# Optimization experiments

Hardware: AMD Instinct MI355X
Metric: run time of the kernel (lower is better)

The kernel has to match this reference:

```python
import jax, jax.numpy as jnp
import numpy as np

IMG = 64
FS = 96
NH = 6          # num_head == channel dim C (forced by LayerNorm(num_head))
B = 8
HW = IMG * IMG  # 4096
FF = FS * FS    # 9216, Mlp in/hidden features
EPS = 1e-5


def setup_inputs() -> dict:
    key = jax.random.key(0)
    ks = jax.random.split(key, 7)
    x = jax.random.normal(ks[0], (B, NH, HW), jnp.float32)
    feature = jax.random.normal(ks[1], (B, NH, FF), jnp.float32)
    s1 = 1.0 / np.sqrt(FF)
    fc1_w = jax.random.uniform(ks[2], (FF, FF), jnp.float32, -s1, s1)
    fc1_b = jax.random.uniform(ks[3], (FF,), jnp.float32, -s1, s1)
    fc2_w = jax.random.uniform(ks[4], (HW, FF), jnp.float32, -s1, s1)
    fc2_b = jax.random.uniform(ks[5], (HW,), jnp.float32, -s1, s1)
    logit_scale = jnp.log(10.0 * jnp.ones((1, 1, HW), jnp.float32))
    norm_w = jnp.ones((NH,), jnp.float32)
    norm_b = jnp.zeros((NH,), jnp.float32)
    return {"x": x, "feature": feature, "fc1_w": fc1_w, "fc1_b": fc1_b,
            "fc2_w": fc2_w, "fc2_b": fc2_b, "logit_scale": logit_scale,
            "norm_w": norm_w, "norm_b": norm_b}


def reference(x, feature, fc1_w, fc1_b, fc2_w, fc2_b, logit_scale, norm_w, norm_b):
    # x: [B, C, HW]; feature: [B, C, FF]
    xt = jnp.swapaxes(x, 1, 2)                                  # [B, HW, C]
    # Mlp (ReLU act, drop=0): FF -> FF -> HW
    h = jax.nn.relu(jnp.einsum('bcf,hf->bch', feature, fc1_w) + fc1_b)
    f = jnp.einsum('bch,oh->bco', h, fc2_w) + fc2_b             # [B, C, HW]
    # cosine-style logit scale, clamped at log(1/0.01)
    max_log = jnp.log(jnp.float32(100.0))
    ls = jnp.exp(jnp.minimum(logit_scale, max_log))             # [1, 1, HW]
    temp = jnp.einsum('bnc,bcm->bnm', xt, f) * ls               # [B, HW, HW]
    temp = jax.nn.softmax(temp, axis=1)                         # softmax over dim 1
    out = jnp.einsum('bnm,bmc->bnc', temp, xt)                  # [B, HW, C]
    # LayerNorm over last dim (C == num_head), biased variance, eps=1e-5
    mu = jnp.mean(out, axis=-1, keepdims=True)
    var = jnp.mean((out - mu) ** 2, axis=-1, keepdims=True)
    out = (out - mu) / jnp.sqrt(var + EPS) * norm_w + norm_b
    return jnp.swapaxes(out, 1, 2)                              # [B, C, HW]
```

## Files before the change

### kernel.cpp

```cpp
#include <hip/hip_runtime.h>
#include <math.h>

#define BATCH 8
#define CH 6
#define HW 4096
#define FF 9216
#define RC 48
#define LOG2E 1.44269504088896340736f
#define LN100 4.6051701859880913680f

__global__ __launch_bounds__(256) void prep_kernel(
    const float* __restrict__ x, const float* __restrict__ feature,
    float* __restrict__ featT, float* __restrict__ xT)
{
    int i = blockIdx.x * 256 + threadIdx.x;
    if (i < FF * RC) {
        int k = i / RC, r = i - k * RC;
        featT[i] = feature[(size_t)r * FF + k];
    } else {
        int t = i - FF * RC;
        if (t < BATCH * HW * CH) {
            int c = t % CH;
            int n = (t / CH) & (HW - 1);
            int b = t / (HW * CH);
            xT[t] = x[((size_t)(b * CH + c)) * HW + n];
        }
    }
}

__global__ __launch_bounds__(256) void gemm48(
    const float* __restrict__ W, const float* __restrict__ AT,
    float* __restrict__ part, int K, int kchunk)
{
    __shared__ float ldsW[32 * 128];
    __shared__ float ldsA[32 * 48];
    const int t = threadIdx.x;
    const int tx = t & 31;
    const int ty = t >> 5;
    const int j0 = blockIdx.x * 128;
    const int kbase = blockIdx.y * kchunk;
    const int ntiles = kchunk >> 5;

    const int wrow = t >> 3;
    const int wk4  = (t & 7) * 4;

    float acc[4][6];
#pragma unroll
    for (int q = 0; q < 4; ++q)
#pragma unroll
        for (int i = 0; i < 6; ++i) acc[q][i] = 0.f;

    for (int tile = 0; tile < ntiles; ++tile) {
        const int kt = kbase + tile * 32;
#pragma unroll
        for (int rnd = 0; rnd < 4; ++rnd) {
            int row = rnd * 32 + wrow;
            float4 v = *(const float4*)(W + (size_t)(j0 + row) * K + kt + wk4);
            float* dst = ldsW + rnd * 32;
            dst[(wk4 + 0) * 128 + (wrow ^ (wk4 + 0))] = v.x;
            dst[(wk4 + 1) * 128 + (wrow ^ (wk4 + 1))] = v.y;
            dst[(wk4 + 2) * 128 + (wrow ^ (wk4 + 2))] = v.z;
            dst[(wk4 + 3) * 128 + (wrow ^ (wk4 + 3))] = v.w;
        }
        {
            const float2* asrc = (const float2*)(AT + (size_t)kt * RC);
            float2* adst = (float2*)ldsA;
            adst[t]       = asrc[t];
            adst[t + 256] = asrc[t + 256];
            adst[t + 512] = asrc[t + 512];
        }
        __syncthreads();
#pragma unroll 4
        for (int k = 0; k < 32; ++k) {
            const float* wr = ldsW + k * 128;
            int js = tx ^ k;
            float w0 = wr[js];
            float w1 = wr[32 + js];
            float w2 = wr[64 + js];
            float w3 = wr[96 + js];
            const float* ar = ldsA + k * RC + 6 * ty;
            float a0 = ar[0], a1 = ar[1], a2 = ar[2];
            float a3 = ar[3], a4 = ar[4], a5 = ar[5];
            acc[0][0] = fmaf(w0, a0, acc[0][0]);
            acc[0][1] = fmaf(w0, a1, acc[0][1]);
            acc[0][2] = fmaf(w0, a2, acc[0][2]);
            acc[0][3] = fmaf(w0, a3, acc[0][3]);
            acc[0][4] = fmaf(w0, a4, acc[0][4]);
            acc[0][5] = fmaf(w0, a5, acc[0][5]);
            acc[1][0] = fmaf(w1, a0, acc[1][0]);
            acc[1][1] = fmaf(w1, a1, acc[1][1]);
            acc[1][2] = fmaf(w1, a2, acc[1][2]);
            acc[1][3] = fmaf(w1, a3, acc[1][3]);
            acc[1][4] = fmaf(w1, a4, acc[1][4]);
            acc[1][5] = fmaf(w1, a5, acc[1][5]);
            acc[2][0] = fmaf(w2, a0, acc[2][0]);
            acc[2][1] = fmaf(w2, a1, acc[2][1]);
            acc[2][2] = fmaf(w2, a2, acc[2][2]);
            acc[2][3] = fmaf(w2, a3, acc[2][3]);
            acc[2][4] = fmaf(w2, a4, acc[2][4]);
            acc[2][5] = fmaf(w2, a5, acc[2][5]);
            acc[3][0] = fmaf(w3, a0, acc[3][0]);
            acc[3][1] = fmaf(w3, a1, acc[3][1]);
            acc[3][2] = fmaf(w3, a2, acc[3][2]);
            acc[3][3] = fmaf(w3, a3, acc[3][3]);
            acc[3][4] = fmaf(w3, a4, acc[3][4]);
            acc[3][5] = fmaf(w3, a5, acc[3][5]);
        }
        __syncthreads();
    }

    const int N = gridDim.x * 128;
    float* base = part + ((size_t)blockIdx.y * N + j0) * RC + 6 * ty;
#pragma unroll
    for (int q = 0; q < 4; ++q) {
        float* dst = base + (size_t)(q * 32 + tx) * RC;
        float2 v0 = make_float2(acc[q][0], acc[q][1]);
        float2 v1 = make_float2(acc[q][2], acc[q][3]);
        float2 v2 = make_float2(acc[q][4], acc[q][5]);
        *(float2*)(dst + 0) = v0;
        *(float2*)(dst + 2) = v1;
        *(float2*)(dst + 4) = v2;
    }
}

__global__ __launch_bounds__(256) void reduce_relu(
    const float* __restrict__ part, const float* __restrict__ bias,
    float* __restrict__ hT, int nchunks)
{
    int i = blockIdx.x * 256 + threadIdx.x;
    const int total = FF * RC;
    if (i >= total) return;
    float s = 0.f;
    for (int c = 0; c < nchunks; ++c) s += part[(size_t)c * total + i];
    int j = i / RC;
    s += bias[j];
    hT[i] = fmaxf(s, 0.f);
}

__global__ __launch_bounds__(256) void reduce_scale(
    const float* __restrict__ part, const float* __restrict__ bias,
    const float* __restrict__ logit_scale, float* __restrict__ fTs, int nchunks)
{
    int i = blockIdx.x * 256 + threadIdx.x;
    const int total = HW * RC;
    if (i >= total) return;
    float s = 0.f;
    for (int c = 0; c < nchunks; ++c) s += part[(size_t)c * total + i];
    int m = i / RC, rc = i - m * RC;
    int b = rc / CH, cc = rc - b * CH;
    float lv = fminf(logit_scale[m], LN100);
    float ls = __builtin_amdgcn_exp2f(lv * LOG2E);
    s = (s + bias[m]) * ls * LOG2E;
    fTs[((size_t)b * HW + m) * CH + cc] = s;
}

__global__ __launch_bounds__(256) void colsum_kernel(
    const float* __restrict__ fTs, const float* __restrict__ xT,
    float* __restrict__ Dpart)
{
    __shared__ float xs[512 * CH];
    const int t = threadIdx.x;
    const int b = blockIdx.y;
    const int ns = blockIdx.z;
    {
        const float4* src = (const float4*)(xT + ((size_t)b * HW + ns * 512) * CH);
        float4* dst = (float4*)xs;
        dst[t]       = src[t];
        dst[t + 256] = src[t + 256];
        dst[t + 512] = src[t + 512];
    }
    __syncthreads();

    int m = blockIdx.x * 256 + t;
    const float2* f2 = (const float2*)(fTs + ((size_t)b * HW + m) * CH);
    float2 fa = f2[0], fb = f2[1], fc = f2[2];
    float s0 = fa.x, s1 = fa.y, s2 = fb.x, s3 = fb.y, s4 = fc.x, s5 = fc.y;

    float D = 0.f;
#pragma unroll 4
    for (int n = 0; n < 512; ++n) {
        const float* xn = xs + n * CH;
        float a = fmaf(s0, xn[0], fmaf(s1, xn[1], fmaf(s2, xn[2],
                  fmaf(s3, xn[3], fmaf(s4, xn[4], s5 * xn[5])))));
        D += __builtin_amdgcn_exp2f(a);
    }
    Dpart[((size_t)b * 8 + ns) * HW + m] = D;
}

__global__ __launch_bounds__(256) void combineD_kernel(
    const float* __restrict__ Dpart, const float* __restrict__ xT,
    float* __restrict__ xR)
{
    int i = blockIdx.x * 256 + threadIdx.x;
    if (i >= BATCH * HW) return;
    int b = i >> 12, m = i & (HW - 1);
    float s = 0.f;
    for (int ns = 0; ns < 8; ++ns) s += Dpart[((size_t)b * 8 + ns) * HW + m];
    float r = 1.0f / s;
    const float2* xs = (const float2*)(xT + (size_t)i * CH);
    float2 v0 = xs[0], v1 = xs[1], v2 = xs[2];
    float2* xd = (float2*)(xR + (size_t)i * CH);
    xd[0] = make_float2(v0.x * r, v0.y * r);
    xd[1] = make_float2(v1.x * r, v1.y * r);
    xd[2] = make_float2(v2.x * r, v2.y * r);
}

__global__ __launch_bounds__(256) void attn_out_kernel(
    const float* __restrict__ fTs, const float* __restrict__ xT,
    const float* __restrict__ xR, const float* __restrict__ nw,
    const float* __restrict__ nb, float* __restrict__ out)
{
    int b = blockIdx.y;
    int wv = threadIdx.x >> 6;
    int lane = threadIdx.x & 63;
    int n0 = (blockIdx.x * 4 + wv) * 8;

    const float* __restrict__ xb = xT + (size_t)b * HW * CH;
    float xn[8][6];
#pragma unroll
    for (int n = 0; n < 8; ++n)
#pragma unroll
        for (int c = 0; c < 6; ++c) xn[n][c] = xb[(size_t)(n0 + n) * CH + c];

    const float* __restrict__ frb = fTs + (size_t)b * HW * CH;
    const float* __restrict__ xrb = xR + (size_t)b * HW * CH;

    float acc[8][6];
#pragma unroll
    for (int n = 0; n < 8; ++n)
#pragma unroll
        for (int c = 0; c < 6; ++c) acc[n][c] = 0.f;

    for (int i = 0; i < 64; ++i) {
        int m = i * 64 + lane;
        const float2* f2 = (const float2*)(frb + (size_t)m * CH);
        float2 fa = f2[0], fb = f2[1], fc = f2[2];
        const float2* x2 = (const float2*)(xrb + (size_t)m * CH);
        float2 xa = x2[0], xb2 = x2[1], xc = x2[2];
        float f0 = fa.x, f1 = fa.y, f2v = fb.x, f3 = fb.y, f4 = fc.x, f5 = fc.y;
#pragma unroll
        for (int n = 0; n < 8; ++n) {
            float a = fmaf(f0, xn[n][0], fmaf(f1, xn[n][1], fmaf(f2v, xn[n][2],
                      fmaf(f3, xn[n][3], fmaf(f4, xn[n][4], f5 * xn[n][5])))));
            float p = __builtin_amdgcn_exp2f(a);
            acc[n][0] = fmaf(p, xa.x, acc[n][0]);
            acc[n][1] = fmaf(p, xa.y, acc[n][1]);
            acc[n][2] = fmaf(p, xb2.x, acc[n][2]);
            acc[n][3] = fmaf(p, xb2.y, acc[n][3]);
            acc[n][4] = fmaf(p, xc.x, acc[n][4]);
            acc[n][5] = fmaf(p, xc.y, acc[n][5]);
        }
    }

#pragma unroll
    for (int n = 0; n < 8; ++n)
#pragma unroll
        for (int c = 0; c < 6; ++c) {
            float v = acc[n][c];
            for (int d = 1; d < 64; d <<= 1) v += __shfl_xor(v, d, 64);
            acc[n][c] = v;
        }

    if (lane == 0) {
        float wc[6], bc[6];
#pragma unroll
        for (int c = 0; c < 6; ++c) { wc[c] = nw[c]; bc[c] = nb[c]; }
#pragma unroll
        for (int n = 0; n < 8; ++n) {
            float mu = (acc[n][0] + acc[n][1] + acc[n][2] +
                        acc[n][3] + acc[n][4] + acc[n][5]) * (1.f / 6.f);
            float var = 0.f;
#pragma unroll
            for (int c = 0; c < 6; ++c) {
                float dv = acc[n][c] - mu;
                var = fmaf(dv, dv, var);
            }
            var *= (1.f / 6.f);
            float inv = rsqrtf(var + 1e-5f);
#pragma unroll
            for (int c = 0; c < 6; ++c)
                out[((size_t)(b * CH + c)) * HW + n0 + n] =
                    (acc[n][c] - mu) * inv * wc[c] + bc[c];
        }
    }
}

extern "C" void kernel_launch(void* const* d_in, const int* in_sizes, int n_in,
                              void* d_out, int out_size, void* d_ws, size_t ws_size,
                              hipStream_t stream)
{
    const float* x           = (const float*)d_in[0];
    const float* feature     = (const float*)d_in[1];
    const float* fc1_w       = (const float*)d_in[2];
    const float* fc1_b       = (const float*)d_in[3];
    const float* fc2_w       = (const float*)d_in[4];
    const float* fc2_b       = (const float*)d_in[5];
    const float* logit_scale = (const float*)d_in[6];
    const float* norm_w      = (const float*)d_in[7];
    const float* norm_b      = (const float*)d_in[8];
    float* out = (float*)d_out;

    float* ws = (float*)d_ws;
    float* featT = ws;
    float* hT    = featT + 442368;
    float* p1    = hT    + 442368;
    float* p2    = p1    + 3538944;
    float* fTs   = p2    + 1572864;
    float* xT    = fTs   + 196608;
    float* Dpart = xT    + 196608;
    float* xR    = Dpart + 262144;

    prep_kernel<<<(442368 + 196608 + 255) / 256, 256, 0, stream>>>(x, feature, featT, xT);
    gemm48<<<dim3(72, 8), 256, 0, stream>>>(fc1_w, featT, p1, FF, 1152);
    reduce_relu<<<(FF * RC + 255) / 256, 256, 0, stream>>>(p1, fc1_b, hT, 8);
    gemm48<<<dim3(32, 8), 256, 0, stream>>>(fc2_w, hT, p2, FF, 1152);
    reduce_scale<<<(HW * RC + 255) / 256, 256, 0, stream>>>(p2, fc2_b, logit_scale, fTs, 8);
    colsum_kernel<<<dim3(16, BATCH, 8), 256, 0, stream>>>(fTs, xT, Dpart);
    combineD_kernel<<<(BATCH * HW + 255) / 256, 256, 0, stream>>>(Dpart, xT, xR);
    attn_out_kernel<<<dim3(128, BATCH), 256, 0, stream>>>(fTs, xT, xR, norm_w, norm_b, out);
}
```

Measured before the change: 806.7 us.

## Replace FP32 FMA GEMMs with split-bf16 MFMA GEMMs for the MLP

Replaces the LDS-tiled FP32 FMA GEMM for both MLP layers with a matrix-core kernel. It uses 16x16x32 bf16 MFMA and a three-term hi/lo bf16 split to keep close to FP32 accuracy. Activations are pre-split into hi/lo bf16 arrays in prep and reduce_relu. Weights are split on the fly from FP32 global loads with no LDS staging. The partial-sum layout changes to row-major per k-chunk, and fc2 uses more k-chunks (24). The aim is to move the dominant weight-streaming GEMMs from VALU onto matrix cores, at the cost of extra split arithmetic, triple MFMA issue and some precision loss.

```diff
diff --git a/kernel.cpp b/kernel.cpp
--- a/kernel.cpp
+++ b/kernel.cpp
@@ -9,14 +9,29 @@
 #define LOG2E 1.44269504088896340736f
 #define LN100 4.6051701859880913680f
 
+typedef unsigned short u16;
+typedef __attribute__((ext_vector_type(4))) float f32x4;
+typedef __attribute__((ext_vector_type(8))) short short8;
+union F8 { uint4 u; short8 b; };
+
+__device__ __forceinline__ void split1(float f, unsigned& h, unsigned& l) {
+    unsigned u = __float_as_uint(f);
+    unsigned hb = (u + 0x8000u) & 0xffff0000u;
+    h = hb >> 16;
+    float r = f - __uint_as_float(hb);
+    l = (__float_as_uint(r) + 0x8000u) >> 16;
+}
+
 __global__ __launch_bounds__(256) void prep_kernel(
     const float* __restrict__ x, const float* __restrict__ feature,
-    float* __restrict__ featT, float* __restrict__ xT)
+    u16* __restrict__ fHi, u16* __restrict__ fLo, float* __restrict__ xT)
 {
     int i = blockIdx.x * 256 + threadIdx.x;
     if (i < FF * RC) {
-        int k = i / RC, r = i - k * RC;
-        featT[i] = feature[(size_t)r * FF + k];
+        unsigned h, l;
+        split1(feature[i], h, l);
+        fHi[i] = (u16)h;
+        fLo[i] = (u16)l;
     } else {
         int t = i - FF * RC;
         if (t < BATCH * HW * CH) {
@@ -28,130 +43,106 @@
     }
 }
 
-__global__ __launch_bounds__(256) void gemm48(
-    const float* __restrict__ W, const float* __restrict__ AT,
-    float* __restrict__ part, int K, int kchunk)
-{
-    __shared__ float ldsW[32 * 128];
-    __shared__ float ldsA[32 * 48];
-    const int t = threadIdx.x;
-    const int tx = t & 31;
-    const int ty = t >> 5;
-    const int j0 = blockIdx.x * 128;
+__global__ __launch_bounds__(128, 4) void gemm_mfma(
+    const float* __restrict__ W, const u16* __restrict__ Ahi,
+    const u16* __restrict__ Alo, float* __restrict__ part,
+    int N, int kchunk)
+{
+    const int lane = threadIdx.x & 63;
+    const int wv = threadIdx.x >> 6;
+    const int col = lane & 15;
+    const int kg = lane >> 4;
+    const int j0 = blockIdx.x * 64 + wv * 32;
     const int kbase = blockIdx.y * kchunk;
     const int ntiles = kchunk >> 5;
 
-    const int wrow = t >> 3;
-    const int wk4  = (t & 7) * 4;
-
-    float acc[4][6];
-#pragma unroll
-    for (int q = 0; q < 4; ++q)
-#pragma unroll
-        for (int i = 0; i < 6; ++i) acc[q][i] = 0.f;
-
-    for (int tile = 0; tile < ntiles; ++tile) {
-        const int kt = kbase + tile * 32;
-#pragma unroll
-        for (int rnd = 0; rnd < 4; ++rnd) {
-            int row = rnd * 32 + wrow;
-            float4 v = *(const float4*)(W + (size_t)(j0 + row) * K + kt + wk4);
-            float* dst = ldsW + rnd * 32;
-            dst[(wk4 + 0) * 128 + (wrow ^ (wk4 + 0))] = v.x;
-            dst[(wk4 + 1) * 128 + (wrow ^ (wk4 + 1))] = v.y;
-            dst[(wk4 + 2) * 128 + (wrow ^ (wk4 + 2))] = v.z;
-            dst[(wk4 + 3) * 128 + (wrow ^ (wk4 + 3))] = v.w;
-        }
-        {
-            const float2* asrc = (const float2*)(AT + (size_t)kt * RC);
-            float2* adst = (float2*)ldsA;
-            adst[t]       = asrc[t];
-            adst[t + 256] = asrc[t + 256];
-            adst[t + 512] = asrc[t + 512];
-        }
-        __syncthreads();
-#pragma unroll 4
-        for (int k = 0; k < 32; ++k) {
-            const float* wr = ldsW + k * 128;
-            int js = tx ^ k;
-            float w0 = wr[js];
-            float w1 = wr[32 + js];
-            float w2 = wr[64 + js];
-            float w3 = wr[96 + js];
-            const float* ar = ldsA + k * RC + 6 * ty;
-            float a0 = ar[0], a1 = ar[1], a2 = ar[2];
-            float a3 = ar[3], a4 = ar[4], a5 = ar[5];
-            acc[0][0] = fmaf(w0, a0, acc[0][0]);
-            acc[0][1] = fmaf(w0, a1, acc[0][1]);
-            acc[0][2] = fmaf(w0, a2, acc[0][2]);
-            acc[0][3] = fmaf(w0, a3, acc[0][3]);
-            acc[0][4] = fmaf(w0, a4, acc[0][4]);
-            acc[0][5] = fmaf(w0, a5, acc[0][5]);
-            acc[1][0] = fmaf(w1, a0, acc[1][0]);
-            acc[1][1] = fmaf(w1, a1, acc[1][1]);
-            acc[1][2] = fmaf(w1, a2, acc[1][2]);
-            acc[1][3] = fmaf(w1, a3, acc[1][3]);
-            acc[1][4] = fmaf(w1, a4, acc[1][4]);
-            acc[1][5] = fmaf(w1, a5, acc[1][5]);
-            acc[2][0] = fmaf(w2, a0, acc[2][0]);
-            acc[2][1] = fmaf(w2, a1, acc[2][1]);
-            acc[2][2] = fmaf(w2, a2, acc[2][2]);
-            acc[2][3] = fmaf(w2, a3, acc[2][3]);
-            acc[2][4] = fmaf(w2, a4, acc[2][4]);
-            acc[2][5] = fmaf(w2, a5, acc[2][5]);
-            acc[3][0] = fmaf(w3, a0, acc[3][0]);
-            acc[3][1] = fmaf(w3, a1, acc[3][1]);
-            acc[3][2] = fmaf(w3, a2, acc[3][2]);
-            acc[3][3] = fmaf(w3, a3, acc[3][3]);
-            acc[3][4] = fmaf(w3, a4, acc[3][4]);
-            acc[3][5] = fmaf(w3, a5, acc[3][5]);
-        }
-        __syncthreads();
-    }
-
-    const int N = gridDim.x * 128;
-    float* base = part + ((size_t)blockIdx.y * N + j0) * RC + 6 * ty;
-#pragma unroll
-    for (int q = 0; q < 4; ++q) {
-        float* dst = base + (size_t)(q * 32 + tx) * RC;
-        float2 v0 = make_float2(acc[q][0], acc[q][1]);
-        float2 v1 = make_float2(acc[q][2], acc[q][3]);
-        float2 v2 = make_float2(acc[q][4], acc[q][5]);
-        *(float2*)(dst + 0) = v0;
-        *(float2*)(dst + 2) = v1;
-        *(float2*)(dst + 4) = v2;
+    f32x4 acc[2][3];
+#pragma unroll
+    for (int jt = 0; jt < 2; ++jt)
+#pragma unroll
+        for (int mt = 0; mt < 3; ++mt)
+            acc[jt][mt] = (f32x4){0.f, 0.f, 0.f, 0.f};
+
+    for (int t = 0; t < ntiles; ++t) {
+        const int ko = kbase + t * 32 + kg * 8;
+        F8 aH[3], aL[3];
+#pragma unroll
+        for (int mt = 0; mt < 3; ++mt) {
+            size_t off = (size_t)(mt * 16 + col) * FF + ko;
+            aH[mt].u = *(const uint4*)(Ahi + off);
+            aL[mt].u = *(const uint4*)(Alo + off);
+        }
+#pragma unroll
+        for (int jt = 0; jt < 2; ++jt) {
+            const float* wp = W + (size_t)(j0 + jt * 16 + col) * FF + ko;
+            float4 w0 = *(const float4*)wp;
+            float4 w1 = *(const float4*)(wp + 4);
+            float f[8] = {w0.x, w0.y, w0.z, w0.w, w1.x, w1.y, w1.z, w1.w};
+            unsigned hh[8], ll[8];
+#pragma unroll
+            for (int e = 0; e < 8; ++e) split1(f[e], hh[e], ll[e]);
+            F8 bH, bL;
+            bH.u = make_uint4(hh[0] | (hh[1] << 16), hh[2] | (hh[3] << 16),
+                              hh[4] | (hh[5] << 16), hh[6] | (hh[7] << 16));
+            bL.u = make_uint4(ll[0] | (ll[1] << 16), ll[2] | (ll[3] << 16),
+                              ll[4] | (ll[5] << 16), ll[6] | (ll[7] << 16));
+#pragma unroll
+            for (int mt = 0; mt < 3; ++mt) {
+                acc[jt][mt] = __builtin_amdgcn_mfma_f32_16x16x32_bf16(
+                    aH[mt].b, bH.b, acc[jt][mt], 0, 0, 0);
+                acc[jt][mt] = __builtin_amdgcn_mfma_f32_16x16x32_bf16(
+                    aH[mt].b, bL.b, acc[jt][mt], 0, 0, 0);
+                acc[jt][mt] = __builtin_amdgcn_mfma_f32_16x16x32_bf16(
+                    aL[mt].b, bH.b, acc[jt][mt], 0, 0, 0);
+            }
+        }
+    }
+
+    const int r0 = (lane >> 4) * 4;
+#pragma unroll
+    for (int jt = 0; jt < 2; ++jt) {
+        int j = j0 + jt * 16 + col;
+#pragma unroll
+        for (int mt = 0; mt < 3; ++mt) {
+            float* dst = part + ((size_t)blockIdx.y * 48 + mt * 16 + r0) * N + j;
+#pragma unroll
+            for (int q = 0; q < 4; ++q) dst[(size_t)q * N] = acc[jt][mt][q];
+        }
     }
 }
 
 __global__ __launch_bounds__(256) void reduce_relu(
     const float* __restrict__ part, const float* __restrict__ bias,
-    float* __restrict__ hT, int nchunks)
+    u16* __restrict__ hHi, u16* __restrict__ hLo)
 {
     int i = blockIdx.x * 256 + threadIdx.x;
-    const int total = FF * RC;
-    if (i >= total) return;
     float s = 0.f;
-    for (int c = 0; c < nchunks; ++c) s += part[(size_t)c * total + i];
-    int j = i / RC;
-    s += bias[j];
-    hT[i] = fmaxf(s, 0.f);
+#pragma unroll
+    for (int c = 0; c < 8; ++c) s += part[(size_t)c * (RC * FF) + i];
+    int j = i % FF;
+    s = fmaxf(s + bias[j], 0.f);
+    unsigned h, l;
+    split1(s, h, l);
+    hHi[i] = (u16)h;
+    hLo[i] = (u16)l;
 }
 
 __global__ __launch_bounds__(256) void reduce_scale(
     const float* __restrict__ part, const float* __restrict__ bias,
-    const float* __restrict__ logit_scale, float* __restrict__ fTs, int nchunks)
+    const float* __restrict__ logit_scale, float* __restrict__ fTs)
 {
     int i = blockIdx.x * 256 + threadIdx.x;
-    const int total = HW * RC;
-    if (i >= total) return;
+    int cc = i % CH;
+    int bm = i / CH;
+    int m = bm & (HW - 1);
+    int b = bm >> 12;
     float s = 0.f;
-    for (int c = 0; c < nchunks; ++c) s += part[(size_t)c * total + i];
-    int m = i / RC, rc = i - m * RC;
-    int b = rc / CH, cc = rc - b * CH;
+#pragma unroll
+    for (int c = 0; c < 24; ++c)
+        s += part[((size_t)c * RC + b * CH + cc) * HW + m];
     float lv = fminf(logit_scale[m], LN100);
     float ls = __builtin_amdgcn_exp2f(lv * LOG2E);
-    s = (s + bias[m]) * ls * LOG2E;
-    fTs[((size_t)b * HW + m) * CH + cc] = s;
+    fTs[i] = (s + bias[m]) * ls * LOG2E;
 }
 
 __global__ __launch_bounds__(256) void colsum_kernel(
@@ -300,21 +291,21 @@
     const float* norm_b      = (const float*)d_in[8];
     float* out = (float*)d_out;
 
-    float* ws = (float*)d_ws;
-    float* featT = ws;
-    float* hT    = featT + 442368;
-    float* p1    = hT    + 442368;
-    float* p2    = p1    + 3538944;
-    float* fTs   = p2    + 1572864;
-    float* xT    = fTs   + 196608;
-    float* Dpart = xT    + 196608;
+    u16* fHi = (u16*)d_ws;
+    u16* fLo = fHi + 442368;
+    u16* hHi = fLo + 442368;
+    u16* hLo = hHi + 442368;
+    float* part = (float*)(hLo + 442368);
+    float* fTs   = part + 4718592;
+    float* xT    = fTs + 196608;
+    float* Dpart = xT + 196608;
     float* xR    = Dpart + 262144;
 
-    prep_kernel<<<(442368 + 196608 + 255) / 256, 256, 0, stream>>>(x, feature, featT, xT);
-    gemm48<<<dim3(72, 8), 256, 0, stream>>>(fc1_w, featT, p1, FF, 1152);
-    reduce_relu<<<(FF * RC + 255) / 256, 256, 0, stream>>>(p1, fc1_b, hT, 8);
-    gemm48<<<dim3(32, 8), 256, 0, stream>>>(fc2_w, hT, p2, FF, 1152);
-    reduce_scale<<<(HW * RC + 255) / 256, 256, 0, stream>>>(p2, fc2_b, logit_scale, fTs, 8);
+    prep_kernel<<<2496, 256, 0, stream>>>(x, feature, fHi, fLo, xT);
+    gemm_mfma<<<dim3(144, 8), 128, 0, stream>>>(fc1_w, fHi, fLo, part, FF, 1152);
+    reduce_relu<<<1728, 256, 0, stream>>>(part, fc1_b, hHi, hLo);
+    gemm_mfma<<<dim3(64, 24), 128, 0, stream>>>(fc2_w, hHi, hLo, part, HW, 384);
+    reduce_scale<<<768, 256, 0, stream>>>(part, fc2_b, logit_scale, fTs);
     colsum_kernel<<<dim3(16, BATCH, 8), 256, 0, stream>>>(fTs, xT, Dpart);
     combineD_kernel<<<(BATCH * HW + 255) / 256, 256, 0, stream>>>(Dpart, xT, xR);
     attn_out_kernel<<<dim3(128, BATCH), 256, 0, stream>>>(fTs, xT, xR, norm_w, norm_b, out);
```

Result: faster. 730.1 us (-9.5%).
